# Kernel optimization log

Measured on AMD Instinct MI355X. Metric: run time of the kernel, lower is better.

## Reference

```python
import jax, jax.numpy as jnp
import numpy as np

N_NODES = 100000
N_EDGES = 3200000
IN_CH, HID_CH, OUT_CH = 128, 128, 64


def setup_inputs() -> dict:
    key = jax.random.key(0)
    k1, k2, k3, k4 = jax.random.split(key, 4)
    x = jax.random.normal(k1, (N_NODES, IN_CH), dtype=jnp.float32)
    edge_index = jax.random.randint(k2, (2, N_EDGES), 0, N_NODES, dtype=jnp.int64)
    # Glorot-ish scaled weights
    W1 = jax.random.normal(k3, (IN_CH, HID_CH), dtype=jnp.float32) / np.sqrt(IN_CH)
    b1 = jnp.zeros((HID_CH,), dtype=jnp.float32)
    W2 = jax.random.normal(k4, (HID_CH, OUT_CH), dtype=jnp.float32) / np.sqrt(HID_CH)
    b2 = jnp.zeros((OUT_CH,), dtype=jnp.float32)
    return {"x": x, "edge_index": edge_index, "W1": W1, "b1": b1, "W2": W2, "b2": b2}


def _gcn_conv(x, src, dst, norm, W, b, n_nodes):
    # Linear transform first (PyG GCNConv order), then normalized scatter-add aggregation.
    h = x @ W                                   # [N, out]
    msg = norm[:, None] * h[src]                # [E_tot, out] gather + per-edge scale
    out = jax.ops.segment_sum(msg, dst, num_segments=n_nodes)
    return out + b


def reference(x, edge_index, W1, b1, W2, b2):
    n = x.shape[0]
    loop = jnp.arange(n, dtype=edge_index.dtype)
    src = jnp.concatenate([edge_index[0], loop])  # add self-loops (GCNConv default)
    dst = jnp.concatenate([edge_index[1], loop])
    # symmetric normalization: deg computed on dst with unit edge weights
    deg = jax.ops.segment_sum(jnp.ones_like(dst, dtype=x.dtype), dst, num_segments=n)
    dinv = jnp.where(deg > 0, jax.lax.rsqrt(deg), 0.0)
    norm = dinv[src] * dinv[dst]                 # [E_tot]
    h = _gcn_conv(x, src, dst, norm, W1, b1, n)
    h = jax.nn.relu(h)
    z = _gcn_conv(h, src, dst, norm, W2, b2, n)
    return z
```

## Files before the change

### kernel.cpp

```cpp
#include <hip/hip_runtime.h>
#include <cstdint>
#include <cstddef>

static __device__ __forceinline__ unsigned int f2bf_rne(float f) {
    unsigned int u = __float_as_uint(f);
    unsigned int r = 0x7FFFu + ((u >> 16) & 1u);
    return (u + r) >> 16;
}
static __device__ __forceinline__ unsigned int pack_bf2(float lo, float hi) {
    return f2bf_rne(lo) | (f2bf_rne(hi) << 16);
}
static __device__ __forceinline__ float bf_lo(unsigned int w) {
    return __uint_as_float(w << 16);
}
static __device__ __forceinline__ float bf_hi(unsigned int w) {
    return __uint_as_float(w & 0xFFFF0000u);
}

#define BKT_CH 16384


__global__ void k_detect64(const unsigned int* ei, int e, int* is64) {
    __shared__ int nonzero;
    if (threadIdx.x == 0) nonzero = 0;
    __syncthreads();
    for (int i = threadIdx.x; i < 4096; i += blockDim.x) {
        size_t k = (size_t)((unsigned long long)i * (unsigned long long)e / 4096ull);
        if (ei[2 * k + 1] != 0u) nonzero = 1;
    }
    __syncthreads();
    if (threadIdx.x == 0) *is64 = nonzero ? 0 : 1;
}

__global__ void k_zero512(int* p) { p[threadIdx.x] = 0; }

__global__ __launch_bounds__(256) void k_hist(const void* ei_raw, int e, const int* is64,
                                              int* __restrict__ bkt_cnt) {
    __shared__ int lcnt[512];
    int t = threadIdx.x;
    for (int j = t; j < 512; j += 256) lcnt[j] = 0;
    __syncthreads();
    int lo = blockIdx.x * BKT_CH;
    int hi = lo + BKT_CH; if (hi > e) hi = e;
    if (*is64) {
        const long long* p = (const long long*)ei_raw;
        for (int i = lo + t; i < hi; i += 256)
            atomicAdd(&lcnt[((int)p[(size_t)e + i]) >> 8], 1);
    } else {
        const int* p = (const int*)ei_raw;
        for (int i = lo + t; i < hi; i += 256)
            atomicAdd(&lcnt[p[(size_t)e + i] >> 8], 1);
    }
    __syncthreads();
    for (int j = t; j < 512; j += 256)
        if (lcnt[j]) atomicAdd(&bkt_cnt[j], lcnt[j]);
}

__global__ __launch_bounds__(512) void k_scan_bkt(const int* __restrict__ bkt_cnt,
                                                  int* __restrict__ bkt_base,
                                                  int* __restrict__ bkt_cursor, int nb) {
    __shared__ int s[512];
    int t = threadIdx.x;
    int v = (t < nb) ? bkt_cnt[t] : 0;
    s[t] = v;
    __syncthreads();
    #pragma unroll
    for (int d = 1; d < 512; d <<= 1) {
        int tmp = (t >= d) ? s[t - d] : 0;
        __syncthreads();
        s[t] += tmp;
        __syncthreads();
    }
    if (t < nb) {
        int b = s[t] - v;
        bkt_base[t]   = b;
        bkt_cursor[t] = b;
    }
    if (t == 511) bkt_base[nb] = s[511];
}

__global__ __launch_bounds__(256) void k_bucket(const void* ei_raw, int e, const int* is64,
                                                int* __restrict__ bkt_cursor,
                                                unsigned long long* __restrict__ pout) {
    __shared__ int lcnt[512];
    __shared__ int lbase[512];
    int t = threadIdx.x;
    int lo = blockIdx.x * BKT_CH;
    int hi = lo + BKT_CH; if (hi > e) hi = e;
    for (int j = t; j < 512; j += 256) lcnt[j] = 0;
    __syncthreads();
    bool w64 = (*is64 != 0);
    const long long* p64 = (const long long*)ei_raw;
    const int*       p32 = (const int*)ei_raw;
    for (int i = lo + t; i < hi; i += 256) {
        int d = w64 ? (int)p64[(size_t)e + i] : p32[(size_t)e + i];
        atomicAdd(&lcnt[d >> 8], 1);
    }
    __syncthreads();
    for (int j = t; j < 512; j += 256) {
        int c = lcnt[j];
        lbase[j] = c ? atomicAdd(&bkt_cursor[j], c) : 0;
        lcnt[j] = 0;
    }
    __syncthreads();
    for (int i = lo + t; i < hi; i += 256) {
        int s, d;
        if (w64) { s = (int)p64[i]; d = (int)p64[(size_t)e + i]; }
        else     { s = p32[i];      d = p32[(size_t)e + i]; }
        int b = d >> 8;
        int pos = lbase[b] + atomicAdd(&lcnt[b], 1);
        pout[pos] = ((unsigned long long)(unsigned int)d << 32) | (unsigned int)s;
    }
}

__global__ __launch_bounds__(256) void k_place_deg(const unsigned long long* __restrict__ pairs,
                                                   const int* __restrict__ bkt_base,
                                                   int n, int nb,
                                                   int* __restrict__ row_ptr,
                                                   float* __restrict__ dinv,
                                                   int* __restrict__ src_sorted) {
    __shared__ int lcnt[256];
    __shared__ int ls[256];
    __shared__ int lcur[256];
    int b = blockIdx.x;
    int t = threadIdx.x;
    int base = bkt_base[b], end = bkt_base[b + 1];
    lcnt[t] = 0;
    __syncthreads();
    for (int i = base + t; i < end; i += 256)
        atomicAdd(&lcnt[(int)(pairs[i] >> 32) & 255], 1);
    __syncthreads();
    int v = lcnt[t];
    ls[t] = v;
    __syncthreads();
    #pragma unroll
    for (int d = 1; d < 256; d <<= 1) {
        int tmp = (t >= d) ? ls[t - d] : 0;
        __syncthreads();
        ls[t] += tmp;
        __syncthreads();
    }
    int nodebase = base + ls[t] - v;
    int node = (b << 8) + t;
    if (node < n) {
        row_ptr[node] = nodebase;
        dinv[node] = rsqrtf((float)(v + 1));
    }
    lcur[t] = nodebase;
    __syncthreads();
    for (int i = base + t; i < end; i += 256) {
        unsigned long long pr = pairs[i];
        int pos = atomicAdd(&lcur[(int)(pr >> 32) & 255], 1);
        src_sorted[pos] = (int)(pr & 0xFFFFFFFFu);
    }
    if (t == 0 && b == nb - 1) row_ptr[n] = end;
}


__global__ __launch_bounds__(256) void k_gemm128(const float* __restrict__ A,
                                                 const float* __restrict__ W,
                                                 const float* __restrict__ dinv,
                                                 unsigned int* __restrict__ hsb, int M) {
    __shared__ float sA[64][36];
    __shared__ float sW[32][128];
    int tid = threadIdx.x;
    int tx = tid & 15;
    int ty = tid >> 4;
    int row0 = blockIdx.x * 64;
    float acc[4][8] = {};
    for (int k0 = 0; k0 < 128; k0 += 32) {
        __syncthreads();
        for (int i = tid; i < 512; i += 256) {
            int r = i >> 3, c4 = i & 7;
            float4 v = {0.f, 0.f, 0.f, 0.f};
            int gr = row0 + r;
            if (gr < M) v = *reinterpret_cast<const float4*>(&A[(size_t)gr * 128 + k0 + c4 * 4]);
            *reinterpret_cast<float4*>(&sA[r][c4 * 4]) = v;
        }
        for (int i = tid; i < 1024; i += 256) {
            int r = i >> 5, c4 = i & 31;
            *reinterpret_cast<float4*>(&sW[r][c4 * 4]) =
                *reinterpret_cast<const float4*>(&W[(size_t)(k0 + r) * 128 + c4 * 4]);
        }
        __syncthreads();
        #pragma unroll
        for (int k = 0; k < 32; k += 4) {
            float4 a[4];
            #pragma unroll
            for (int r = 0; r < 4; ++r)
                a[r] = *reinterpret_cast<const float4*>(&sA[ty * 4 + r][k]);
            #pragma unroll
            for (int kk = 0; kk < 4; ++kk) {
                float4 w0 = *reinterpret_cast<const float4*>(&sW[k + kk][tx * 8]);
                float4 w1 = *reinterpret_cast<const float4*>(&sW[k + kk][tx * 8 + 4]);
                #pragma unroll
                for (int r = 0; r < 4; ++r) {
                    float av = (&a[r].x)[kk];
                    acc[r][0] += av * w0.x; acc[r][1] += av * w0.y;
                    acc[r][2] += av * w0.z; acc[r][3] += av * w0.w;
                    acc[r][4] += av * w1.x; acc[r][5] += av * w1.y;
                    acc[r][6] += av * w1.z; acc[r][7] += av * w1.w;
                }
            }
        }
    }
    #pragma unroll
    for (int r = 0; r < 4; ++r) {
        int gr = row0 + ty * 4 + r;
        if (gr < M) {
            float di = dinv[gr];
            uint4 o;
            o.x = pack_bf2(acc[r][0] * di, acc[r][1] * di);
            o.y = pack_bf2(acc[r][2] * di, acc[r][3] * di);
            o.z = pack_bf2(acc[r][4] * di, acc[r][5] * di);
            o.w = pack_bf2(acc[r][6] * di, acc[r][7] * di);
            *reinterpret_cast<uint4*>(&hsb[(size_t)gr * 64 + tx * 4]) = o;
        }
    }
}

__global__ __launch_bounds__(256) void k_gemm64(const float* __restrict__ A,
                                                const float* __restrict__ W,
                                                const float* __restrict__ dinv,
                                                unsigned int* __restrict__ zsb, int M) {
    __shared__ float sA[64][36];
    __shared__ float sW[32][64];
    int tid = threadIdx.x;
    int tx = tid & 15;
    int ty = tid >> 4;
    int row0 = blockIdx.x * 64;
    float acc[4][4] = {};
    for (int k0 = 0; k0 < 128; k0 += 32) {
        __syncthreads();
        for (int i = tid; i < 512; i += 256) {
            int r = i >> 3, c4 = i & 7;
            float4 v = {0.f, 0.f, 0.f, 0.f};
            int gr = row0 + r;
            if (gr < M) v = *reinterpret_cast<const float4*>(&A[(size_t)gr * 128 + k0 + c4 * 4]);
            *reinterpret_cast<float4*>(&sA[r][c4 * 4]) = v;
        }
        for (int i = tid; i < 512; i += 256) {
            int r = i >> 4, c4 = i & 15;
            *reinterpret_cast<float4*>(&sW[r][c4 * 4]) =
                *reinterpret_cast<const float4*>(&W[(size_t)(k0 + r) * 64 + c4 * 4]);
        }
        __syncthreads();
        #pragma unroll
        for (int k = 0; k < 32; k += 4) {
            float4 a[4];
            #pragma unroll
            for (int r = 0; r < 4; ++r)
                a[r] = *reinterpret_cast<const float4*>(&sA[ty * 4 + r][k]);
            #pragma unroll
            for (int kk = 0; kk < 4; ++kk) {
                float4 w = *reinterpret_cast<const float4*>(&sW[k + kk][tx * 4]);
                #pragma unroll
                for (int r = 0; r < 4; ++r) {
                    float av = (&a[r].x)[kk];
                    acc[r][0] += av * w.x; acc[r][1] += av * w.y;
                    acc[r][2] += av * w.z; acc[r][3] += av * w.w;
                }
            }
        }
    }
    #pragma unroll
    for (int r = 0; r < 4; ++r) {
        int gr = row0 + ty * 4 + r;
        if (gr < M) {
            float di = dinv[gr];
            uint2 o;
            o.x = pack_bf2(acc[r][0] * di, acc[r][1] * di);
            o.y = pack_bf2(acc[r][2] * di, acc[r][3] * di);
            *reinterpret_cast<uint2*>(&zsb[(size_t)gr * 32 + tx * 2]) = o;
        }
    }
}


__global__ __launch_bounds__(64) void k_agg1(const unsigned int* __restrict__ hsb,
                                             const float* __restrict__ dinv,
                                             const int* __restrict__ row_ptr,
                                             const int* __restrict__ src_sorted,
                                             const float* __restrict__ b1,
                                             float* __restrict__ h2) {
    int i = blockIdx.x;
    int c = threadIdx.x;
    unsigned int w = hsb[(size_t)i * 64 + c];
    float ax = bf_lo(w), ay = bf_hi(w);
    int lo = row_ptr[i], hi = row_ptr[i + 1];
    int e = lo;
    for (; e + 8 <= hi; e += 8) {
        int s0 = src_sorted[e + 0], s1 = src_sorted[e + 1];
        int s2 = src_sorted[e + 2], s3 = src_sorted[e + 3];
        int s4 = src_sorted[e + 4], s5 = src_sorted[e + 5];
        int s6 = src_sorted[e + 6], s7 = src_sorted[e + 7];
        unsigned int w0 = hsb[(size_t)s0 * 64 + c];
        unsigned int w1 = hsb[(size_t)s1 * 64 + c];
        unsigned int w2 = hsb[(size_t)s2 * 64 + c];
        unsigned int w3 = hsb[(size_t)s3 * 64 + c];
        unsigned int w4 = hsb[(size_t)s4 * 64 + c];
        unsigned int w5 = hsb[(size_t)s5 * 64 + c];
        unsigned int w6 = hsb[(size_t)s6 * 64 + c];
        unsigned int w7 = hsb[(size_t)s7 * 64 + c];
        ax += ((bf_lo(w0) + bf_lo(w1)) + (bf_lo(w2) + bf_lo(w3)))
            + ((bf_lo(w4) + bf_lo(w5)) + (bf_lo(w6) + bf_lo(w7)));
        ay += ((bf_hi(w0) + bf_hi(w1)) + (bf_hi(w2) + bf_hi(w3)))
            + ((bf_hi(w4) + bf_hi(w5)) + (bf_hi(w6) + bf_hi(w7)));
    }
    if (e + 4 <= hi) {
        int s0 = src_sorted[e + 0], s1 = src_sorted[e + 1];
        int s2 = src_sorted[e + 2], s3 = src_sorted[e + 3];
        unsigned int w0 = hsb[(size_t)s0 * 64 + c];
        unsigned int w1 = hsb[(size_t)s1 * 64 + c];
        unsigned int w2 = hsb[(size_t)s2 * 64 + c];
        unsigned int w3 = hsb[(size_t)s3 * 64 + c];
        ax += (bf_lo(w0) + bf_lo(w1)) + (bf_lo(w2) + bf_lo(w3));
        ay += (bf_hi(w0) + bf_hi(w1)) + (bf_hi(w2) + bf_hi(w3));
        e += 4;
    }
    for (; e < hi; ++e) {
        int s = src_sorted[e];
        unsigned int ws = hsb[(size_t)s * 64 + c];
        ax += bf_lo(ws);
        ay += bf_hi(ws);
    }
    float di = dinv[i];
    float2 bb = *reinterpret_cast<const float2*>(&b1[2 * c]);
    float v0 = di * ax + bb.x;
    float v1 = di * ay + bb.y;
    float2 o = {v0 > 0.f ? v0 : 0.f, v1 > 0.f ? v1 : 0.f};
    *reinterpret_cast<float2*>(&h2[(size_t)i * 128 + 2 * c]) = o;
}

__global__ __launch_bounds__(64) void k_agg2(const unsigned int* __restrict__ zsb,
                                             const float* __restrict__ dinv,
                                             const int* __restrict__ row_ptr,
                                             const int* __restrict__ src_sorted,
                                             const float* __restrict__ b2,
                                             float* __restrict__ out, int n) {
    int i = blockIdx.x * 2 + (threadIdx.x >> 5);
    int c = threadIdx.x & 31;
    if (i >= n) return;
    unsigned int w = zsb[(size_t)i * 32 + c];
    float ax = bf_lo(w), ay = bf_hi(w);
    int lo = row_ptr[i], hi = row_ptr[i + 1];
    int e = lo;
    for (; e + 8 <= hi; e += 8) {
        int s0 = src_sorted[e + 0], s1 = src_sorted[e + 1];
        int s2 = src_sorted[e + 2], s3 = src_sorted[e + 3];
        int s4 = src_sorted[e + 4], s5 = src_sorted[e + 5];
        int s6 = src_sorted[e + 6], s7 = src_sorted[e + 7];
        unsigned int w0 = zsb[(size_t)s0 * 32 + c];
        unsigned int w1 = zsb[(size_t)s1 * 32 + c];
        unsigned int w2 = zsb[(size_t)s2 * 32 + c];
        unsigned int w3 = zsb[(size_t)s3 * 32 + c];
        unsigned int w4 = zsb[(size_t)s4 * 32 + c];
        unsigned int w5 = zsb[(size_t)s5 * 32 + c];
        unsigned int w6 = zsb[(size_t)s6 * 32 + c];
        unsigned int w7 = zsb[(size_t)s7 * 32 + c];
        ax += ((bf_lo(w0) + bf_lo(w1)) + (bf_lo(w2) + bf_lo(w3)))
            + ((bf_lo(w4) + bf_lo(w5)) + (bf_lo(w6) + bf_lo(w7)));
        ay += ((bf_hi(w0) + bf_hi(w1)) + (bf_hi(w2) + bf_hi(w3)))
            + ((bf_hi(w4) + bf_hi(w5)) + (bf_hi(w6) + bf_hi(w7)));
    }
    if (e + 4 <= hi) {
        int s0 = src_sorted[e + 0], s1 = src_sorted[e + 1];
        int s2 = src_sorted[e + 2], s3 = src_sorted[e + 3];
        unsigned int w0 = zsb[(size_t)s0 * 32 + c];
        unsigned int w1 = zsb[(size_t)s1 * 32 + c];
        unsigned int w2 = zsb[(size_t)s2 * 32 + c];
        unsigned int w3 = zsb[(size_t)s3 * 32 + c];
        ax += (bf_lo(w0) + bf_lo(w1)) + (bf_lo(w2) + bf_lo(w3));
        ay += (bf_hi(w0) + bf_hi(w1)) + (bf_hi(w2) + bf_hi(w3));
        e += 4;
    }
    for (; e < hi; ++e) {
        int s = src_sorted[e];
        unsigned int ws = zsb[(size_t)s * 32 + c];
        ax += bf_lo(ws);
        ay += bf_hi(ws);
    }
    float di = dinv[i];
    float2 bb = *reinterpret_cast<const float2*>(&b2[2 * c]);
    float2 o = {di * ax + bb.x, di * ay + bb.y};
    *reinterpret_cast<float2*>(&out[(size_t)i * 64 + 2 * c]) = o;
}


static inline size_t alignup(size_t v) { return (v + 255) & ~(size_t)255; }

extern "C" void kernel_launch(void* const* d_in, const int* in_sizes, int n_in,
                              void* d_out, int out_size, void* d_ws, size_t ws_size,
                              hipStream_t stream) {
    const float* x  = (const float*)d_in[0];
    const void*  ei = d_in[1];
    const float* W1 = (const float*)d_in[2];
    const float* b1 = (const float*)d_in[3];
    const float* W2 = (const float*)d_in[4];
    const float* b2 = (const float*)d_in[5];

    const int n = in_sizes[0] / 128;
    const int e = in_sizes[1] / 2;

    char* p = (char*)d_ws;
    auto take = [&](size_t bytes) { char* q = p; p += alignup(bytes); return q; };
    size_t pairs_bytes = (size_t)e * 8;
    size_t hsb_bytes   = (size_t)n * 64 * 4;
    size_t regA_bytes  = pairs_bytes > hsb_bytes ? pairs_bytes : hsb_bytes;
    char* regA = (char*)take(regA_bytes);
    unsigned long long* pairs = (unsigned long long*)regA;
    unsigned int*       hsb   = (unsigned int*)regA;

    float*        h2         = (float*)take((size_t)n * 128 * 4);
    int*          is64       = (int*)  take(4);
    float*        dinv       = (float*)take((size_t)n * 4);
    int*          row_ptr    = (int*)  take((size_t)(n + 1) * 4);
    int*          bkt_cnt    = (int*)  take(512 * 4);
    int*          bkt_base   = (int*)  take(513 * 4);
    int*          bkt_cursor = (int*)  take(512 * 4);
    int*          src_sorted = (int*)  take((size_t)e * 4);
    unsigned int* zsb        = (unsigned int*)take((size_t)n * 32 * 4);
    if ((size_t)(p - (char*)d_ws) > ws_size) return;

    const int nb_bkt  = (n + 255) >> 8;
    const int nb_chnk = (e + BKT_CH - 1) / BKT_CH;

    k_detect64<<<1, 256, 0, stream>>>((const unsigned int*)ei, e, is64);
    k_zero512<<<1, 512, 0, stream>>>(bkt_cnt);
    k_hist<<<nb_chnk, 256, 0, stream>>>(ei, e, is64, bkt_cnt);
    k_scan_bkt<<<1, 512, 0, stream>>>(bkt_cnt, bkt_base, bkt_cursor, nb_bkt);
    k_bucket<<<nb_chnk, 256, 0, stream>>>(ei, e, is64, bkt_cursor, pairs);
    k_place_deg<<<nb_bkt, 256, 0, stream>>>(pairs, bkt_base, n, nb_bkt,
                                            row_ptr, dinv, src_sorted);

    k_gemm128<<<(n + 63) / 64, 256, 0, stream>>>(x, W1, dinv, hsb, n);
    k_agg1<<<n, 64, 0, stream>>>(hsb, dinv, row_ptr, src_sorted, b1, h2);
    k_gemm64<<<(n + 63) / 64, 256, 0, stream>>>(h2, W2, dinv, zsb, n);
    k_agg2<<<(n + 1) / 2, 64, 0, stream>>>(zsb, dinv, row_ptr, src_sorted, b2, (float*)d_out, n);
}
```

Before: 363.9 us.

## Shrink intermediate traffic: packed 32-bit bucket pairs, bf16 hidden layer, LDS-staged bucketing

The bucketing kernel now stages each chunk's src/dst in shared memory, so edge indices are read from global memory once instead of twice. It writes 32-bit packed entries (local dst byte plus 24-bit src) instead of 64-bit pairs, which halves the pairs buffer. The layer-1 output h2 is stored as packed bf16 and expanded inside the second GEMM, halving that round trip, and src_sorted reads use nontemporal loads. The risks are lower occupancy from the 64KB of shared memory, src values limited to 24 bits, and extra precision loss from the bf16 hidden activations.

```diff
diff --git a/kernel.cpp b/kernel.cpp
--- a/kernel.cpp
+++ b/kernel.cpp
@@ -17,7 +17,7 @@
     return __uint_as_float(w & 0xFFFF0000u);
 }
 
-#define BKT_CH 16384
+#define BKT_CH 8192
 
 
 __global__ void k_detect64(const unsigned int* ei, int e, int* is64) {
@@ -81,19 +81,27 @@
 
 __global__ __launch_bounds__(256) void k_bucket(const void* ei_raw, int e, const int* is64,
                                                 int* __restrict__ bkt_cursor,
-                                                unsigned long long* __restrict__ pout) {
+                                                unsigned int* __restrict__ pout) {
+    __shared__ int ldst[BKT_CH];
+    __shared__ int lsrc[BKT_CH];
     __shared__ int lcnt[512];
     __shared__ int lbase[512];
     int t = threadIdx.x;
     int lo = blockIdx.x * BKT_CH;
     int hi = lo + BKT_CH; if (hi > e) hi = e;
+    int m = hi - lo;
     for (int j = t; j < 512; j += 256) lcnt[j] = 0;
     __syncthreads();
     bool w64 = (*is64 != 0);
     const long long* p64 = (const long long*)ei_raw;
     const int*       p32 = (const int*)ei_raw;
-    for (int i = lo + t; i < hi; i += 256) {
-        int d = w64 ? (int)p64[(size_t)e + i] : p32[(size_t)e + i];
+    for (int idx = t; idx < m; idx += 256) {
+        size_t i = (size_t)lo + idx;
+        int s, d;
+        if (w64) { s = (int)p64[i]; d = (int)p64[(size_t)e + i]; }
+        else     { s = p32[i];      d = p32[(size_t)e + i]; }
+        ldst[idx] = d;
+        lsrc[idx] = s;
         atomicAdd(&lcnt[d >> 8], 1);
     }
     __syncthreads();
@@ -103,17 +111,15 @@
         lcnt[j] = 0;
     }
     __syncthreads();
-    for (int i = lo + t; i < hi; i += 256) {
-        int s, d;
-        if (w64) { s = (int)p64[i]; d = (int)p64[(size_t)e + i]; }
-        else     { s = p32[i];      d = p32[(size_t)e + i]; }
+    for (int idx = t; idx < m; idx += 256) {
+        int d = ldst[idx], s = lsrc[idx];
         int b = d >> 8;
         int pos = lbase[b] + atomicAdd(&lcnt[b], 1);
-        pout[pos] = ((unsigned long long)(unsigned int)d << 32) | (unsigned int)s;
-    }
-}
-
-__global__ __launch_bounds__(256) void k_place_deg(const unsigned long long* __restrict__ pairs,
+        pout[pos] = ((unsigned int)(d & 255) << 24) | (unsigned int)s;
+    }
+}
+
+__global__ __launch_bounds__(256) void k_place_deg(const unsigned int* __restrict__ pairs,
                                                    const int* __restrict__ bkt_base,
                                                    int n, int nb,
                                                    int* __restrict__ row_ptr,
@@ -128,7 +134,7 @@
     lcnt[t] = 0;
     __syncthreads();
     for (int i = base + t; i < end; i += 256)
-        atomicAdd(&lcnt[(int)(pairs[i] >> 32) & 255], 1);
+        atomicAdd(&lcnt[__builtin_nontemporal_load(&pairs[i]) >> 24], 1);
     __syncthreads();
     int v = lcnt[t];
     ls[t] = v;
@@ -149,9 +155,9 @@
     lcur[t] = nodebase;
     __syncthreads();
     for (int i = base + t; i < end; i += 256) {
-        unsigned long long pr = pairs[i];
-        int pos = atomicAdd(&lcur[(int)(pr >> 32) & 255], 1);
-        src_sorted[pos] = (int)(pr & 0xFFFFFFFFu);
+        unsigned int pr = __builtin_nontemporal_load(&pairs[i]);
+        int pos = atomicAdd(&lcur[pr >> 24], 1);
+        src_sorted[pos] = (int)(pr & 0x00FFFFFFu);
     }
     if (t == 0 && b == nb - 1) row_ptr[n] = end;
 }
@@ -219,7 +225,7 @@
     }
 }
 
-__global__ __launch_bounds__(256) void k_gemm64(const float* __restrict__ A,
+__global__ __launch_bounds__(256) void k_gemm64(const unsigned int* __restrict__ Ab,
                                                 const float* __restrict__ W,
                                                 const float* __restrict__ dinv,
                                                 unsigned int* __restrict__ zsb, int M) {
@@ -232,12 +238,12 @@
     float acc[4][4] = {};
     for (int k0 = 0; k0 < 128; k0 += 32) {
         __syncthreads();
-        for (int i = tid; i < 512; i += 256) {
-            int r = i >> 3, c4 = i & 7;
-            float4 v = {0.f, 0.f, 0.f, 0.f};
+        for (int i = tid; i < 1024; i += 256) {
+            int r = i >> 4, w = i & 15;
             int gr = row0 + r;
-            if (gr < M) v = *reinterpret_cast<const float4*>(&A[(size_t)gr * 128 + k0 + c4 * 4]);
-            *reinterpret_cast<float4*>(&sA[r][c4 * 4]) = v;
+            unsigned int pv = (gr < M) ? Ab[(size_t)gr * 64 + (k0 >> 1) + w] : 0u;
+            sA[r][2 * w]     = bf_lo(pv);
+            sA[r][2 * w + 1] = bf_hi(pv);
         }
         for (int i = tid; i < 512; i += 256) {
             int r = i >> 4, c4 = i & 15;
@@ -282,7 +288,7 @@
                                              const int* __restrict__ row_ptr,
                                              const int* __restrict__ src_sorted,
                                              const float* __restrict__ b1,
-                                             float* __restrict__ h2) {
+                                             unsigned int* __restrict__ h2b) {
     int i = blockIdx.x;
     int c = threadIdx.x;
     unsigned int w = hsb[(size_t)i * 64 + c];
@@ -290,10 +296,14 @@
     int lo = row_ptr[i], hi = row_ptr[i + 1];
     int e = lo;
     for (; e + 8 <= hi; e += 8) {
-        int s0 = src_sorted[e + 0], s1 = src_sorted[e + 1];
-        int s2 = src_sorted[e + 2], s3 = src_sorted[e + 3];
-        int s4 = src_sorted[e + 4], s5 = src_sorted[e + 5];
-        int s6 = src_sorted[e + 6], s7 = src_sorted[e + 7];
+        int s0 = __builtin_nontemporal_load(&src_sorted[e + 0]);
+        int s1 = __builtin_nontemporal_load(&src_sorted[e + 1]);
+        int s2 = __builtin_nontemporal_load(&src_sorted[e + 2]);
+        int s3 = __builtin_nontemporal_load(&src_sorted[e + 3]);
+        int s4 = __builtin_nontemporal_load(&src_sorted[e + 4]);
+        int s5 = __builtin_nontemporal_load(&src_sorted[e + 5]);
+        int s6 = __builtin_nontemporal_load(&src_sorted[e + 6]);
+        int s7 = __builtin_nontemporal_load(&src_sorted[e + 7]);
         unsigned int w0 = hsb[(size_t)s0 * 64 + c];
         unsigned int w1 = hsb[(size_t)s1 * 64 + c];
         unsigned int w2 = hsb[(size_t)s2 * 64 + c];
@@ -308,8 +318,10 @@
             + ((bf_hi(w4) + bf_hi(w5)) + (bf_hi(w6) + bf_hi(w7)));
     }
     if (e + 4 <= hi) {
-        int s0 = src_sorted[e + 0], s1 = src_sorted[e + 1];
-        int s2 = src_sorted[e + 2], s3 = src_sorted[e + 3];
+        int s0 = __builtin_nontemporal_load(&src_sorted[e + 0]);
+        int s1 = __builtin_nontemporal_load(&src_sorted[e + 1]);
+        int s2 = __builtin_nontemporal_load(&src_sorted[e + 2]);
+        int s3 = __builtin_nontemporal_load(&src_sorted[e + 3]);
         unsigned int w0 = hsb[(size_t)s0 * 64 + c];
         unsigned int w1 = hsb[(size_t)s1 * 64 + c];
         unsigned int w2 = hsb[(size_t)s2 * 64 + c];
@@ -319,7 +331,7 @@
         e += 4;
     }
     for (; e < hi; ++e) {
-        int s = src_sorted[e];
+        int s = __builtin_nontemporal_load(&src_sorted[e]);
         unsigned int ws = hsb[(size_t)s * 64 + c];
         ax += bf_lo(ws);
         ay += bf_hi(ws);
@@ -328,8 +340,8 @@
     float2 bb = *reinterpret_cast<const float2*>(&b1[2 * c]);
     float v0 = di * ax + bb.x;
     float v1 = di * ay + bb.y;
-    float2 o = {v0 > 0.f ? v0 : 0.f, v1 > 0.f ? v1 : 0.f};
-    *reinterpret_cast<float2*>(&h2[(size_t)i * 128 + 2 * c]) = o;
+    unsigned int pv = pack_bf2(v0 > 0.f ? v0 : 0.f, v1 > 0.f ? v1 : 0.f);
+    __builtin_nontemporal_store(pv, &h2b[(size_t)i * 64 + c]);
 }
 
 __global__ __launch_bounds__(64) void k_agg2(const unsigned int* __restrict__ zsb,
@@ -346,10 +358,14 @@
     int lo = row_ptr[i], hi = row_ptr[i + 1];
     int e = lo;
     for (; e + 8 <= hi; e += 8) {
-        int s0 = src_sorted[e + 0], s1 = src_sorted[e + 1];
-        int s2 = src_sorted[e + 2], s3 = src_sorted[e + 3];
-        int s4 = src_sorted[e + 4], s5 = src_sorted[e + 5];
-        int s6 = src_sorted[e + 6], s7 = src_sorted[e + 7];
+        int s0 = __builtin_nontemporal_load(&src_sorted[e + 0]);
+        int s1 = __builtin_nontemporal_load(&src_sorted[e + 1]);
+        int s2 = __builtin_nontemporal_load(&src_sorted[e + 2]);
+        int s3 = __builtin_nontemporal_load(&src_sorted[e + 3]);
+        int s4 = __builtin_nontemporal_load(&src_sorted[e + 4]);
+        int s5 = __builtin_nontemporal_load(&src_sorted[e + 5]);
+        int s6 = __builtin_nontemporal_load(&src_sorted[e + 6]);
+        int s7 = __builtin_nontemporal_load(&src_sorted[e + 7]);
         unsigned int w0 = zsb[(size_t)s0 * 32 + c];
         unsigned int w1 = zsb[(size_t)s1 * 32 + c];
         unsigned int w2 = zsb[(size_t)s2 * 32 + c];
@@ -364,8 +380,10 @@
             + ((bf_hi(w4) + bf_hi(w5)) + (bf_hi(w6) + bf_hi(w7)));
     }
     if (e + 4 <= hi) {
-        int s0 = src_sorted[e + 0], s1 = src_sorted[e + 1];
-        int s2 = src_sorted[e + 2], s3 = src_sorted[e + 3];
+        int s0 = __builtin_nontemporal_load(&src_sorted[e + 0]);
+        int s1 = __builtin_nontemporal_load(&src_sorted[e + 1]);
+        int s2 = __builtin_nontemporal_load(&src_sorted[e + 2]);
+        int s3 = __builtin_nontemporal_load(&src_sorted[e + 3]);
         unsigned int w0 = zsb[(size_t)s0 * 32 + c];
         unsigned int w1 = zsb[(size_t)s1 * 32 + c];
         unsigned int w2 = zsb[(size_t)s2 * 32 + c];
@@ -375,7 +393,7 @@
         e += 4;
     }
     for (; e < hi; ++e) {
-        int s = src_sorted[e];
+        int s = __builtin_nontemporal_load(&src_sorted[e]);
         unsigned int ws = zsb[(size_t)s * 32 + c];
         ax += bf_lo(ws);
         ay += bf_hi(ws);
@@ -404,14 +422,14 @@
 
     char* p = (char*)d_ws;
     auto take = [&](size_t bytes) { char* q = p; p += alignup(bytes); return q; };
-    size_t pairs_bytes = (size_t)e * 8;
+    size_t pairs_bytes = (size_t)e * 4;
     size_t hsb_bytes   = (size_t)n * 64 * 4;
     size_t regA_bytes  = pairs_bytes > hsb_bytes ? pairs_bytes : hsb_bytes;
     char* regA = (char*)take(regA_bytes);
-    unsigned long long* pairs = (unsigned long long*)regA;
-    unsigned int*       hsb   = (unsigned int*)regA;
-
-    float*        h2         = (float*)take((size_t)n * 128 * 4);
+    unsigned int* pairs = (unsigned int*)regA;
+    unsigned int* hsb   = (unsigned int*)regA;
+
+    unsigned int* h2b        = (unsigned int*)take((size_t)n * 64 * 4);
     int*          is64       = (int*)  take(4);
     float*        dinv       = (float*)take((size_t)n * 4);
     int*          row_ptr    = (int*)  take((size_t)(n + 1) * 4);
@@ -434,7 +452,7 @@
                                             row_ptr, dinv, src_sorted);
 
     k_gemm128<<<(n + 63) / 64, 256, 0, stream>>>(x, W1, dinv, hsb, n);
-    k_agg1<<<n, 64, 0, stream>>>(hsb, dinv, row_ptr, src_sorted, b1, h2);
-    k_gemm64<<<(n + 63) / 64, 256, 0, stream>>>(h2, W2, dinv, zsb, n);
+    k_agg1<<<n, 64, 0, stream>>>(hsb, dinv, row_ptr, src_sorted, b1, h2b);
+    k_gemm64<<<(n + 63) / 64, 256, 0, stream>>>(h2b, W2, dinv, zsb, n);
     k_agg2<<<(n + 1) / 2, 64, 0, stream>>>(zsb, dinv, row_ptr, src_sorted, b2, (float*)d_out, n);
 }
```

Measured after the change: 353.9 us. -2.8%, faster.
